# Performance work log

Hardware: AMD Instinct MI355X
Metric: run time of the kernel (lower is better)

The kernel has to match this reference:

```python
import jax, jax.numpy as jnp
from jax import lax
import numpy as np

GAMMA, ALPHA, BETA, THETA = 0.5, 0.5, 1.0, 1.0
BLOCK = 512  # tile size over the p2 point dim for the streaming K=1 knn


def _min_sqdist(p1, p2):
    """K=1 knn_points: min squared distance from each p1 point to p2. (B,N1,3),(B,N2,3) -> (B,N1).
    Streams p2 in blocks with a running min, never materializing the full NxM matrix."""
    B, N2, _ = p2.shape
    nb = N2 // BLOCK
    p2b = jnp.transpose(p2.reshape(B, nb, BLOCK, 3), (1, 0, 2, 3))  # (nb,B,BLOCK,3)
    p1sq = jnp.sum(p1 * p1, axis=-1)  # (B,N1)

    def step(carry, chunk):
        # ||a-b||^2 = ||a||^2 - 2 a.b + ||b||^2
        d = (p1sq[:, :, None]
             - 2.0 * jnp.einsum('bnd,bmd->bnm', p1, chunk)
             + jnp.sum(chunk * chunk, axis=-1)[:, None, :])
        return jnp.minimum(carry, jnp.min(d, axis=-1)), None

    init = jnp.full(p1sq.shape, jnp.inf, dtype=p1.dtype)
    out, _ = lax.scan(step, init, p2b)
    return out


def _pnt2quat(grasp_pred):
    center = grasp_pred[..., :3]
    q = grasp_pred[..., 3:]
    q = q / jnp.sqrt(jnp.sum(q * q, axis=-1, keepdims=True) + 1e-12)
    return center, q


def _mat2quat(g):
    R = g[..., :3, :3]
    t = g[..., :3, 3]
    tr = R[..., 0, 0] + R[..., 1, 1] + R[..., 2, 2]
    w = 0.5 * jnp.sqrt(jnp.maximum(1.0 + tr, 1e-12))
    inv4w = 1.0 / (4.0 * w)
    x = (R[..., 2, 1] - R[..., 1, 2]) * inv4w
    y = (R[..., 0, 2] - R[..., 2, 0]) * inv4w
    z = (R[..., 1, 0] - R[..., 0, 1]) * inv4w
    q = jnp.stack([w, x, y, z], axis=-1)
    return t, q


def setup_inputs() -> dict:
    key = jax.random.key(0)
    ks = jax.random.split(key, 8)
    B, N, M = 4, 16384, 2048
    xyz = jax.random.normal(ks[0], (B, N, 3), dtype=jnp.float32)
    sample_xyz = jax.random.normal(ks[1], (B, M, 3), dtype=jnp.float32)
    temp = jnp.asarray(0.5, dtype=jnp.float32)
    grasp_pred = jax.random.normal(ks[2], (B, M, 7), dtype=jnp.float32)
    # build valid SE(3) ground-truth grasps: rotation from unit quaternion (w>=0) + translation
    q = jax.random.normal(ks[3], (B, M, 4), dtype=jnp.float32)
    q = q / jnp.sqrt(jnp.sum(q * q, axis=-1, keepdims=True) + 1e-12)
    q = jnp.where(q[..., :1] < 0, -q, q)
    w, x, y, z = q[..., 0], q[..., 1], q[..., 2], q[..., 3]
    R = jnp.stack([
        jnp.stack([1 - 2 * (y * y + z * z), 2 * (x * y - w * z), 2 * (x * z + w * y)], -1),
        jnp.stack([2 * (x * y + w * z), 1 - 2 * (x * x + z * z), 2 * (y * z - w * x)], -1),
        jnp.stack([2 * (x * z - w * y), 2 * (y * z + w * x), 1 - 2 * (x * x + y * y)], -1),
    ], -2)  # (B,M,3,3)
    t = jax.random.normal(ks[4], (B, M, 3), dtype=jnp.float32)
    top = jnp.concatenate([R, t[..., None]], axis=-1)  # (B,M,3,4)
    bottom = jnp.broadcast_to(jnp.array([0., 0., 0., 1.], jnp.float32), (B, M, 1, 4))
    grasp_gt = jnp.concatenate([top, bottom], axis=-2)  # (B,M,4,4)
    class_pred = jax.random.uniform(ks[5], (B, M), dtype=jnp.float32, minval=1e-4, maxval=1.0 - 1e-4)
    class_gt = (jax.random.uniform(ks[6], (B, M)) < 0.5).astype(jnp.float32)
    return {"xyz": xyz, "sample_xyz": sample_xyz, "temp": temp, "grasp_pred": grasp_pred,
            "grasp_gt": grasp_gt, "class_pred": class_pred, "class_gt": class_gt}


def reference(xyz, sample_xyz, temp, grasp_pred, grasp_gt, class_pred, class_gt):
    # sample loss (chamfer-style with K=1 knn in both directions + max-min coverage term)
    d_smp_org = _min_sqdist(sample_xyz, xyz)   # (B,M)
    d_org_smp = _min_sqdist(xyz, sample_xyz)   # (B,N)
    sample_loss = (jnp.mean(d_smp_org)
                   + jnp.mean(jnp.max(d_smp_org, axis=-1))
                   + GAMMA * jnp.mean(d_org_smp))
    # projection loss
    proj_loss = temp ** 2
    center_pred, quat_pred = _pnt2quat(grasp_pred)
    center_gt, quat_gt = _mat2quat(grasp_gt)
    cls_w = class_gt.reshape(-1)
    dist = jnp.linalg.norm(center_pred.reshape(-1, 3) - center_gt.reshape(-1, 3) + 1e-6, axis=-1)
    trans_loss = jnp.mean(dist * cls_w)
    dot = jnp.sum(quat_pred.reshape(-1, 4) * quat_gt.reshape(-1, 4), axis=-1)
    rot = jnp.arccos(jnp.clip(jnp.abs(dot), 0.0, 1.0 - 1e-7))
    rot_loss = jnp.mean(rot * cls_w)
    reg_loss = trans_loss + ALPHA * rot_loss
    # classification loss (BCE on probabilities)
    p = jnp.clip(class_pred, 1e-7, 1.0 - 1e-7)
    cls_loss = -jnp.mean(class_gt * jnp.log(p) + (1.0 - class_gt) * jnp.log(1.0 - p))
    return THETA * sample_loss + proj_loss + BETA * reg_loss + cls_loss
```

## Files before the change

kernel.cpp:

```cpp
#include <hip/hip_runtime.h>
#include <math.h>

#define BB 4
#define NN 16384
#define MM 2048
#define BM (BB*MM)
#define BN (BB*NN)
#define CHUNK 512

#define ACCOFF (BM+BN)
#define WS_FLOATS (ACCOFF+9)

__global__ __launch_bounds__(256) void k_init(unsigned int* __restrict__ ws) {
    int i = blockIdx.x * 256 + threadIdx.x;
    if (i < ACCOFF) ws[i] = 0x7F800000u;
    else if (i < WS_FLOATS) ws[i] = 0u;
}

__global__ __launch_bounds__(256) void k_min(const float* __restrict__ xyz,
                                             const float* __restrict__ smp,
                                             unsigned int* __restrict__ ws) {
    __shared__ float4 tgt[CHUNK];
    const int tid = threadIdx.x;
    const int bx  = blockIdx.x;
    const float* qptr;
    const float* tptr;
    unsigned int* outp;
    if (bx < 256) {
        int qb = bx >> 5;
        int nc = bx & 31;
        int b  = qb >> 1;
        int qbase = b * MM + (qb & 1) * 1024;
        qptr = smp + (size_t)qbase * 3;
        tptr = xyz + (size_t)(b * NN + nc * CHUNK) * 3;
        outp = ws + qbase;
    } else {
        int bx2 = bx - 256;
        int qb = bx2 >> 2;
        int mc = bx2 & 3;
        int b  = qb >> 4;
        int qbase = b * NN + (qb & 15) * 1024;
        qptr = xyz + (size_t)qbase * 3;
        tptr = smp + (size_t)(b * MM + mc * CHUNK) * 3;
        outp = ws + BM + qbase;
    }
    for (int p = tid; p < CHUNK; p += 256) {
        float x = tptr[3*p+0], y = tptr[3*p+1], z = tptr[3*p+2];
        tgt[p] = make_float4(-2.0f*x, -2.0f*y, -2.0f*z, x*x + y*y + z*z);
    }
    float qx[4], qy[4], qz[4], qsq[4], mn[4];
#pragma unroll
    for (int k = 0; k < 4; ++k) {
        int q = tid + k * 256;
        qx[k] = qptr[3*q+0]; qy[k] = qptr[3*q+1]; qz[k] = qptr[3*q+2];
        qsq[k] = qx[k]*qx[k] + qy[k]*qy[k] + qz[k]*qz[k];
        mn[k] = INFINITY;
    }
    __syncthreads();
#pragma unroll 4
    for (int j = 0; j < CHUNK; ++j) {
        float4 t = tgt[j];
#pragma unroll
        for (int k = 0; k < 4; ++k) {
            float d = fmaf(t.x, qx[k], fmaf(t.y, qy[k], fmaf(t.z, qz[k], t.w)));
            mn[k] = fminf(mn[k], d);
        }
    }
#pragma unroll
    for (int k = 0; k < 4; ++k) {
        float v = fmaxf(mn[k] + qsq[k], 0.0f);
        atomicMin(outp + tid + k * 256, __float_as_uint(v));
    }
}

__device__ __forceinline__ float blockSum256(float v, volatile float* s4) {
#pragma unroll
    for (int o = 32; o > 0; o >>= 1) v += __shfl_down(v, o, 64);
    int lane = threadIdx.x & 63, w = threadIdx.x >> 6;
    if (lane == 0) s4[w] = v;
    __syncthreads();
    return s4[0] + s4[1] + s4[2] + s4[3];
}

__device__ __forceinline__ float blockMax256(float v, volatile float* s4) {
#pragma unroll
    for (int o = 32; o > 0; o >>= 1) v = fmaxf(v, __shfl_down(v, o, 64));
    int lane = threadIdx.x & 63, w = threadIdx.x >> 6;
    if (lane == 0) s4[w] = v;
    __syncthreads();
    return fmaxf(fmaxf(s4[0], s4[1]), fmaxf(s4[2], s4[3]));
}

__global__ __launch_bounds__(256) void k_reduce(const float* __restrict__ gp,
                                                const float* __restrict__ gg,
                                                const float* __restrict__ cp,
                                                const float* __restrict__ cg,
                                                unsigned int* __restrict__ ws) {
    __shared__ float s4a[4], s4b[4], s4c[4];
    float* wsf = (float*)ws;
    float* acc = wsf + ACCOFF;
    int bx = blockIdx.x, tid = threadIdx.x;
    if (bx < 32) {
        int i = bx * 256 + tid;
        float v = wsf[i];
        float s  = blockSum256(v, s4a);
        float mx = blockMax256(v, s4b);
        if (tid == 0) {
            atomicAdd(&acc[0], s);
            atomicMax((unsigned int*)acc + 1 + (bx >> 3), __float_as_uint(mx));
        }
    } else if (bx < 288) {
        int i = (bx - 32) * 256 + tid;
        float v = wsf[BM + i];
        float s = blockSum256(v, s4a);
        if (tid == 0) atomicAdd(&acc[5], s);
    } else {
        int m = (bx - 288) * 256 + tid;
        const float* g = gp + (size_t)m * 7;
        float cxp = g[0], cyp = g[1], czp = g[2];
        float q0 = g[3], q1 = g[4], q2 = g[5], q3 = g[6];
        float invq = 1.0f / sqrtf(q0*q0 + q1*q1 + q2*q2 + q3*q3 + 1e-12f);
        const float* G = gg + (size_t)m * 16;
        float tr = G[0] + G[5] + G[10];
        float w = 0.5f * sqrtf(fmaxf(1.0f + tr, 1e-12f));
        float inv4w = 1.0f / (4.0f * w);
        float gqx = (G[9] - G[6]) * inv4w;
        float gqy = (G[2] - G[8]) * inv4w;
        float gqz = (G[4] - G[1]) * inv4w;
        float cw = cg[m];
        float dx = cxp - G[3]  + 1e-6f;
        float dy = cyp - G[7]  + 1e-6f;
        float dz = czp - G[11] + 1e-6f;
        float dist = sqrtf(dx*dx + dy*dy + dz*dz);
        float dot = (q0*w + q1*gqx + q2*gqy + q3*gqz) * invq;
        float rot = acosf(fminf(fabsf(dot), 1.0f - 1e-7f));
        float p = fminf(fmaxf(cp[m], 1e-7f), 1.0f - 1e-7f);
        float ce = cw * logf(p) + (1.0f - cw) * logf(1.0f - p);
        float s1 = blockSum256(dist * cw, s4a);
        float s2 = blockSum256(rot  * cw, s4b);
        float s3 = blockSum256(ce, s4c);
        if (tid == 0) {
            atomicAdd(&acc[6], s1);
            atomicAdd(&acc[7], s2);
            atomicAdd(&acc[8], s3);
        }
    }
}

__global__ void k_final(const float* __restrict__ temp,
                        unsigned int* __restrict__ ws,
                        float* __restrict__ out) {
    float* acc = (float*)ws + ACCOFF;
    float sample = acc[0] * (1.0f / BM)
                 + (acc[1] + acc[2] + acc[3] + acc[4]) * 0.25f
                 + 0.5f * acc[5] * (1.0f / BN);
    float reg = acc[6] * (1.0f / BM) + 0.5f * acc[7] * (1.0f / BM);
    float cls = -acc[8] * (1.0f / BM);
    float t = temp[0];
    out[0] = sample + t * t + reg + cls;
}

extern "C" void kernel_launch(void* const* d_in, const int* in_sizes, int n_in,
                              void* d_out, int out_size, void* d_ws, size_t ws_size,
                              hipStream_t stream) {
    const float* xyz  = (const float*)d_in[0];
    const float* smp  = (const float*)d_in[1];
    const float* temp = (const float*)d_in[2];
    const float* gp   = (const float*)d_in[3];
    const float* gg   = (const float*)d_in[4];
    const float* cp   = (const float*)d_in[5];
    const float* cg   = (const float*)d_in[6];
    unsigned int* ws  = (unsigned int*)d_ws;
    float* out = (float*)d_out;

    hipLaunchKernelGGL(k_init,   dim3((WS_FLOATS + 255) / 256), dim3(256), 0, stream, ws);
    hipLaunchKernelGGL(k_min,    dim3(512), dim3(256), 0, stream, xyz, smp, ws);
    hipLaunchKernelGGL(k_reduce, dim3(320), dim3(256), 0, stream, gp, gg, cp, cg, ws);
    hipLaunchKernelGGL(k_final,  dim3(1), dim3(1), 0, stream, temp, ws, out);
}
```

Before: 98.07 us.

## Replace atomic min/accumulators with partial buffers and drop init kernel

Each k_min block now writes its partial minima to a separate slot per target split instead of using atomicMin, so the workspace no longer needs an init kernel. k_reduce takes the min across splits and writes per-block partial sums, and k_final reduces them with 256 threads. This removes a launch and the atomic contention. In exchange, each thread holds fewer queries, which means more LDS reads per FMA, and the reduction reads more memory.

```diff
diff --git a/kernel.cpp b/kernel.cpp
--- a/kernel.cpp
+++ b/kernel.cpp
@@ -6,76 +6,71 @@
 #define MM 2048
 #define BM (BB*MM)
 #define BN (BB*NN)
-#define CHUNK 512
 
-#define ACCOFF (BM+BN)
-#define WS_FLOATS (ACCOFF+9)
+#define TGT 1024
+#define QPB 512
+#define S1  16
+#define S2  2
 
-__global__ __launch_bounds__(256) void k_init(unsigned int* __restrict__ ws) {
-    int i = blockIdx.x * 256 + threadIdx.x;
-    if (i < ACCOFF) ws[i] = 0x7F800000u;
-    else if (i < WS_FLOATS) ws[i] = 0u;
-}
+#define PART1OFF 0
+#define PART2OFF (S1*BM)
+#define REDOFF   (PART1OFF + S1*BM + S2*BN)
+#define R_SUMS1  (REDOFF)
+#define R_MAXES  (REDOFF+8)
+#define R_SUMS2  (REDOFF+16)
+#define R_GST    (REDOFF+80)
+#define R_GSR    (REDOFF+112)
+#define R_GSC    (REDOFF+144)
 
 __global__ __launch_bounds__(256) void k_min(const float* __restrict__ xyz,
                                              const float* __restrict__ smp,
-                                             unsigned int* __restrict__ ws) {
-    __shared__ float4 tgt[CHUNK];
+                                             float* __restrict__ ws) {
+    __shared__ float4 tgt[TGT];
     const int tid = threadIdx.x;
     const int bx  = blockIdx.x;
-    const float* qptr;
-    const float* tptr;
-    unsigned int* outp;
+    const float* qptr; const float* tptr; float* outp;
     if (bx < 256) {
-        int qb = bx >> 5;
-        int nc = bx & 31;
-        int b  = qb >> 1;
-        int qbase = b * MM + (qb & 1) * 1024;
-        qptr = smp + (size_t)qbase * 3;
-        tptr = xyz + (size_t)(b * NN + nc * CHUNK) * 3;
-        outp = ws + qbase;
+        int qb = bx >> 1, s = bx & 1;
+        int gq = qb * QPB;
+        int b  = gq >> 14;
+        qptr = xyz + (size_t)gq * 3;
+        tptr = smp + (size_t)(b * MM + s * TGT) * 3;
+        outp = ws + PART2OFF + s * BN + gq;
     } else {
         int bx2 = bx - 256;
-        int qb = bx2 >> 2;
-        int mc = bx2 & 3;
-        int b  = qb >> 4;
-        int qbase = b * NN + (qb & 15) * 1024;
-        qptr = xyz + (size_t)qbase * 3;
-        tptr = smp + (size_t)(b * MM + mc * CHUNK) * 3;
-        outp = ws + BM + qbase;
+        int qb = bx2 >> 4, s = bx2 & 15;
+        int gq = qb * QPB;
+        int b  = gq >> 11;
+        qptr = smp + (size_t)gq * 3;
+        tptr = xyz + (size_t)(b * NN + s * TGT) * 3;
+        outp = ws + PART1OFF + s * BM + gq;
     }
-    for (int p = tid; p < CHUNK; p += 256) {
-        float x = tptr[3*p+0], y = tptr[3*p+1], z = tptr[3*p+2];
+    for (int p = tid; p < TGT; p += 256) {
+        float x = tptr[3*p], y = tptr[3*p+1], z = tptr[3*p+2];
         tgt[p] = make_float4(-2.0f*x, -2.0f*y, -2.0f*z, x*x + y*y + z*z);
     }
-    float qx[4], qy[4], qz[4], qsq[4], mn[4];
-#pragma unroll
-    for (int k = 0; k < 4; ++k) {
-        int q = tid + k * 256;
-        qx[k] = qptr[3*q+0]; qy[k] = qptr[3*q+1]; qz[k] = qptr[3*q+2];
-        qsq[k] = qx[k]*qx[k] + qy[k]*qy[k] + qz[k]*qz[k];
-        mn[k] = INFINITY;
-    }
+    float qx0 = qptr[3*tid],       qy0 = qptr[3*tid+1],       qz0 = qptr[3*tid+2];
+    float qx1 = qptr[3*(tid+256)], qy1 = qptr[3*(tid+256)+1], qz1 = qptr[3*(tid+256)+2];
+    float mn0 = INFINITY, mn1 = INFINITY;
     __syncthreads();
 #pragma unroll 4
-    for (int j = 0; j < CHUNK; ++j) {
-        float4 t = tgt[j];
-#pragma unroll
-        for (int k = 0; k < 4; ++k) {
-            float d = fmaf(t.x, qx[k], fmaf(t.y, qy[k], fmaf(t.z, qz[k], t.w)));
-            mn[k] = fminf(mn[k], d);
-        }
+    for (int j = 0; j < TGT; j += 2) {
+        float4 ta = tgt[j], tb = tgt[j+1];
+        float d0a = fmaf(ta.x, qx0, fmaf(ta.y, qy0, fmaf(ta.z, qz0, ta.w)));
+        float d0b = fmaf(tb.x, qx0, fmaf(tb.y, qy0, fmaf(tb.z, qz0, tb.w)));
+        mn0 = fminf(mn0, fminf(d0a, d0b));
+        float d1a = fmaf(ta.x, qx1, fmaf(ta.y, qy1, fmaf(ta.z, qz1, ta.w)));
+        float d1b = fmaf(tb.x, qx1, fmaf(tb.y, qy1, fmaf(tb.z, qz1, tb.w)));
+        mn1 = fminf(mn1, fminf(d1a, d1b));
     }
-#pragma unroll
-    for (int k = 0; k < 4; ++k) {
-        float v = fmaxf(mn[k] + qsq[k], 0.0f);
-        atomicMin(outp + tid + k * 256, __float_as_uint(v));
-    }
+    outp[tid]       = mn0 + (qx0*qx0 + qy0*qy0 + qz0*qz0);
+    outp[tid + 256] = mn1 + (qx1*qx1 + qy1*qy1 + qz1*qz1);
 }
 
 __device__ __forceinline__ float blockSum256(float v, volatile float* s4) {
 #pragma unroll
     for (int o = 32; o > 0; o >>= 1) v += __shfl_down(v, o, 64);
+    __syncthreads();
     int lane = threadIdx.x & 63, w = threadIdx.x >> 6;
     if (lane == 0) s4[w] = v;
     __syncthreads();
@@ -85,6 +80,7 @@
 __device__ __forceinline__ float blockMax256(float v, volatile float* s4) {
 #pragma unroll
     for (int o = 32; o > 0; o >>= 1) v = fmaxf(v, __shfl_down(v, o, 64));
+    __syncthreads();
     int lane = threadIdx.x & 63, w = threadIdx.x >> 6;
     if (lane == 0) s4[w] = v;
     __syncthreads();
@@ -95,27 +91,34 @@
                                                 const float* __restrict__ gg,
                                                 const float* __restrict__ cp,
                                                 const float* __restrict__ cg,
-                                                unsigned int* __restrict__ ws) {
+                                                float* __restrict__ ws) {
     __shared__ float s4a[4], s4b[4], s4c[4];
-    float* wsf = (float*)ws;
-    float* acc = wsf + ACCOFF;
-    int bx = blockIdx.x, tid = threadIdx.x;
-    if (bx < 32) {
-        int i = bx * 256 + tid;
-        float v = wsf[i];
-        float s  = blockSum256(v, s4a);
-        float mx = blockMax256(v, s4b);
-        if (tid == 0) {
-            atomicAdd(&acc[0], s);
-            atomicMax((unsigned int*)acc + 1 + (bx >> 3), __float_as_uint(mx));
+    const int bx = blockIdx.x, tid = threadIdx.x;
+    if (bx < 8) {
+        float s = 0.0f, mx = -INFINITY;
+#pragma unroll
+        for (int k = 0; k < 4; ++k) {
+            int q = bx * 1024 + tid + k * 256;
+            float v = INFINITY;
+#pragma unroll
+            for (int sp = 0; sp < S1; ++sp) v = fminf(v, ws[PART1OFF + sp * BM + q]);
+            s += v; mx = fmaxf(mx, v);
         }
-    } else if (bx < 288) {
-        int i = (bx - 32) * 256 + tid;
-        float v = wsf[BM + i];
-        float s = blockSum256(v, s4a);
-        if (tid == 0) atomicAdd(&acc[5], s);
+        float bs = blockSum256(s, s4a);
+        float bm = blockMax256(mx, s4b);
+        if (tid == 0) { ws[R_SUMS1 + bx] = bs; ws[R_MAXES + bx] = bm; }
+    } else if (bx < 72) {
+        int i = bx - 8;
+        float s = 0.0f;
+#pragma unroll
+        for (int k = 0; k < 4; ++k) {
+            int q = i * 1024 + tid + k * 256;
+            s += fminf(ws[PART2OFF + q], ws[PART2OFF + BN + q]);
+        }
+        float bs = blockSum256(s, s4a);
+        if (tid == 0) ws[R_SUMS2 + i] = bs;
     } else {
-        int m = (bx - 288) * 256 + tid;
+        int m = (bx - 72) * 256 + tid;
         const float* g = gp + (size_t)m * 7;
         float cxp = g[0], cyp = g[1], czp = g[2];
         float q0 = g[3], q1 = g[4], q2 = g[5], q3 = g[6];
@@ -139,25 +142,35 @@
         float s1 = blockSum256(dist * cw, s4a);
         float s2 = blockSum256(rot  * cw, s4b);
         float s3 = blockSum256(ce, s4c);
-        if (tid == 0) {
-            atomicAdd(&acc[6], s1);
-            atomicAdd(&acc[7], s2);
-            atomicAdd(&acc[8], s3);
-        }
+        int i = bx - 72;
+        if (tid == 0) { ws[R_GST + i] = s1; ws[R_GSR + i] = s2; ws[R_GSC + i] = s3; }
     }
 }
 
-__global__ void k_final(const float* __restrict__ temp,
-                        unsigned int* __restrict__ ws,
-                        float* __restrict__ out) {
-    float* acc = (float*)ws + ACCOFF;
-    float sample = acc[0] * (1.0f / BM)
-                 + (acc[1] + acc[2] + acc[3] + acc[4]) * 0.25f
-                 + 0.5f * acc[5] * (1.0f / BN);
-    float reg = acc[6] * (1.0f / BM) + 0.5f * acc[7] * (1.0f / BM);
-    float cls = -acc[8] * (1.0f / BM);
-    float t = temp[0];
-    out[0] = sample + t * t + reg + cls;
+__global__ __launch_bounds__(256) void k_final(const float* __restrict__ temp,
+                                               const float* __restrict__ ws,
+                                               float* __restrict__ out) {
+    __shared__ float s4[4];
+    const int tid = threadIdx.x;
+    float a = (tid < 8)  ? ws[R_SUMS1 + tid] : 0.0f;
+    float f = (tid < 4)  ? fmaxf(ws[R_MAXES + 2*tid], ws[R_MAXES + 2*tid + 1]) : 0.0f;
+    float b = (tid < 64) ? ws[R_SUMS2 + tid] : 0.0f;
+    float c = (tid < 32) ? ws[R_GST + tid] : 0.0f;
+    float d = (tid < 32) ? ws[R_GSR + tid] : 0.0f;
+    float e = (tid < 32) ? ws[R_GSC + tid] : 0.0f;
+    float A = blockSum256(a, s4);
+    float F = blockSum256(f, s4);
+    float B = blockSum256(b, s4);
+    float C = blockSum256(c, s4);
+    float D = blockSum256(d, s4);
+    float E = blockSum256(e, s4);
+    if (tid == 0) {
+        float sample = A * (1.0f / BM) + F * 0.25f + 0.5f * B * (1.0f / BN);
+        float reg    = C * (1.0f / BM) + 0.5f * D * (1.0f / BM);
+        float cls    = -E * (1.0f / BM);
+        float t = temp[0];
+        out[0] = sample + t * t + reg + cls;
+    }
 }
 
 extern "C" void kernel_launch(void* const* d_in, const int* in_sizes, int n_in,
@@ -170,11 +183,10 @@
     const float* gg   = (const float*)d_in[4];
     const float* cp   = (const float*)d_in[5];
     const float* cg   = (const float*)d_in[6];
-    unsigned int* ws  = (unsigned int*)d_ws;
+    float* ws  = (float*)d_ws;
     float* out = (float*)d_out;
 
-    hipLaunchKernelGGL(k_init,   dim3((WS_FLOATS + 255) / 256), dim3(256), 0, stream, ws);
     hipLaunchKernelGGL(k_min,    dim3(512), dim3(256), 0, stream, xyz, smp, ws);
-    hipLaunchKernelGGL(k_reduce, dim3(320), dim3(256), 0, stream, gp, gg, cp, cg, ws);
-    hipLaunchKernelGGL(k_final,  dim3(1), dim3(1), 0, stream, temp, ws, out);
+    hipLaunchKernelGGL(k_reduce, dim3(104), dim3(256), 0, stream, gp, gg, cp, cg, ws);
+    hipLaunchKernelGGL(k_final,  dim3(1),   dim3(256), 0, stream, temp, ws, out);
 }
```

Result: no change. 98.31 us (+0.2%).
